# Performance work log

Hardware: AMD Instinct MI355X
Metric: run time of the kernel (lower is better)

The kernel has to match this reference:

```python
import jax, jax.numpy as jnp
import numpy as np
import math

B, T, C, H = 2, 2048, 1024, 16
HD = C // H
WINDOW = 256  # local_attn_ctx with attnblocksize=1


def setup_inputs() -> dict:
    key = jax.random.key(0)
    k1, k2, k3 = jax.random.split(key, 3)
    x = jax.random.normal(k1, (B, T, C), dtype=jnp.float32)
    Wqkv = jax.random.normal(k2, (C, 3 * C), dtype=jnp.float32) * 0.02
    bqkv = jnp.zeros((3 * C,), dtype=jnp.float32)
    Wproj = jax.random.normal(k3, (C, C), dtype=jnp.float32) * 0.02
    bproj = jnp.zeros((C,), dtype=jnp.float32)
    # 'local' block-sparse layout at token granularity: causal + sliding window
    i = np.arange(T)[:, None]
    j = np.arange(T)[None, :]
    mask = ((j <= i) & (i - j <= WINDOW)).astype(np.int32)
    return {"x": x, "Wqkv": Wqkv, "bqkv": bqkv, "Wproj": Wproj, "bproj": bproj,
            "mask": jnp.asarray(mask)}


def reference(x, Wqkv, bqkv, Wproj, bproj, mask):
    Bb, Tt, Cc = x.shape
    qkv = (x @ Wqkv + bqkv).reshape(Bb, Tt, 3, H, HD)  # [B,T,3,H,hd]
    q = jnp.transpose(qkv[:, :, 0], (0, 2, 1, 3))  # [B,H,T,hd]
    k = jnp.transpose(qkv[:, :, 1], (0, 2, 1, 3))
    v = jnp.transpose(qkv[:, :, 2], (0, 2, 1, 3))
    scale = 1.0 / math.sqrt(HD)
    att = jnp.einsum('bhqd,bhkd->bhqk', q, k) * scale  # dense T x T scores
    att = jnp.where(mask[:Tt, :Tt] == 0, -jnp.inf, att)
    att = jax.nn.softmax(att, axis=-1)
    y = jnp.einsum('bhqk,bhkd->bhqd', att, v)
    y = jnp.transpose(y, (0, 2, 1, 3)).reshape(Bb, Tt, Cc)
    return y @ Wproj + bproj
```

## Files before the change

### kernel.cpp

```cpp
#include <hip/hip_runtime.h>
#include <hip/hip_bf16.h>
#include <math.h>

typedef __bf16 bf16;
typedef __attribute__((ext_vector_type(8))) __bf16 bf16x8;
typedef __attribute__((ext_vector_type(4))) __bf16 bf16x4;
typedef __attribute__((ext_vector_type(4))) float f32x4;

#define B_  2
#define T_  2048
#define C_  1024
#define H_  16
#define HD_ 64
#define WIN_ 256

#define GLOAD16(g, l)                                                        \
  __builtin_amdgcn_global_load_lds(                                          \
      (const __attribute__((address_space(1))) void*)(g),                    \
      (__attribute__((address_space(3))) void*)(l), 16, 0, 0)

__device__ inline void bar() {
  asm volatile("" ::: "memory");
  __builtin_amdgcn_s_barrier();
  asm volatile("" ::: "memory");
}


__global__ __launch_bounds__(256) void cvt_f32_bf16_k(const float* __restrict__ in,
                                                      bf16* __restrict__ out) {
  int idx = blockIdx.x * 256 + threadIdx.x;
  const float4 v = ((const float4*)in)[idx];
  bf16x4 o;
  o[0] = (bf16)v.x; o[1] = (bf16)v.y; o[2] = (bf16)v.z; o[3] = (bf16)v.w;
  ((bf16x4*)out)[idx] = o;
}

__global__ __launch_bounds__(256) void transpose_cvt_k(const float* __restrict__ W,
                                                       bf16* __restrict__ WT,
                                                       int K, int N) {
  __shared__ float t[32][33];
  int n0 = blockIdx.x * 32, k0 = blockIdx.y * 32;
  int tx = threadIdx.x, ty = threadIdx.y;
  #pragma unroll
  for (int i = 0; i < 32; i += 8)
    t[ty + i][tx] = W[(size_t)(k0 + ty + i) * N + (n0 + tx)];
  __syncthreads();
  #pragma unroll
  for (int i = 0; i < 32; i += 8)
    WT[(size_t)(n0 + ty + i) * K + (k0 + tx)] = (bf16)t[tx][ty + i];
}


template <int MODE>
__global__ __launch_bounds__(512, 2) void gemm8p_k(const bf16* __restrict__ A,
                                                   const bf16* __restrict__ Bt,
                                                   const float* __restrict__ bias,
                                                   void* __restrict__ out0,
                                                   void* __restrict__ out1,
                                                   int M, int N, int K) {
  const int bm = blockIdx.x * 256;
  const int bn = blockIdx.y * 256;
  const int tid  = threadIdx.x;
  const int wid  = tid >> 6;
  const int lane = tid & 63;
  const int wr = wid >> 2;
  const int wc = wid & 3;
  const int lr = lane & 15;
  const int g  = lane >> 4;

  __shared__ bf16 As[2][256 * 64];
  __shared__ bf16 Bs[2][256 * 64];

  f32x4 acc[8][4] = {};

  const int sr = lane >> 3;
  const int sc = ((lane & 7) ^ sr) << 3;
  const bf16* aS = A  + (size_t)(bm + wid * 8 + sr) * K + sc;
  const bf16* bS = Bt + (size_t)(bn + wid * 8 + sr) * K + sc;

  #define STA(p_, q_, u_)                                                    \
    GLOAD16(aS + (size_t)((q_) * 64) * K + (u_) * 64,                        \
            &As[p_][((q_) * 64 + wid * 8) * 64])
  #define STB(p_, q_, u_)                                                    \
    GLOAD16(bS + (size_t)((q_) * 64) * K + (u_) * 64,                        \
            &Bs[p_][((q_) * 64 + wid * 8) * 64])

  const int NT  = K >> 6;
  const int kc0 = ((g    ) ^ (lr & 7)) << 3;
  const int kc1 = ((4 + g) ^ (lr & 7)) << 3;

  STA(0, 0, 0); STA(0, 2, 0); STA(0, 1, 0); STA(0, 3, 0);
  STB(0, 0, 0); STB(0, 1, 0); STB(0, 2, 0); STB(0, 3, 0);
  STA(1, 0, 1); STA(1, 2, 1);
  asm volatile("s_waitcnt vmcnt(2)" ::: "memory");
  __builtin_amdgcn_s_barrier();
  asm volatile("" ::: "memory");

  #define MFMA16(mb, a0_, a1_, a2_, a3_)                                     \
    do {                                                                     \
      __builtin_amdgcn_s_setprio(1);                                         \
      _Pragma("unroll")                                                      \
      for (int n = 0; n < 4; ++n) {                                          \
        acc[(mb) + 0][n] = __builtin_amdgcn_mfma_f32_16x16x32_bf16(a0_, bv[n], acc[(mb) + 0][n], 0, 0, 0); \
        acc[(mb) + 1][n] = __builtin_amdgcn_mfma_f32_16x16x32_bf16(a1_, bv[n], acc[(mb) + 1][n], 0, 0, 0); \
        acc[(mb) + 2][n] = __builtin_amdgcn_mfma_f32_16x16x32_bf16(a2_, bv[n], acc[(mb) + 2][n], 0, 0, 0); \
        acc[(mb) + 3][n] = __builtin_amdgcn_mfma_f32_16x16x32_bf16(a3_, bv[n], acc[(mb) + 3][n], 0, 0, 0); \
      }                                                                      \
      __builtin_amdgcn_s_setprio(0);                                         \
    } while (0)

  for (int u = 0; u < NT; ++u) {
    const int p  = u & 1;
    const int pn = p ^ 1;
    const bf16* Ar = &As[p][(wr * 128 + lr) * 64];
    const bf16* Br = &Bs[p][(wc * 64  + lr) * 64];
    bf16x8 bv[4], a0, a1, a2, a3;

    #pragma unroll
    for (int n = 0; n < 4; ++n) bv[n] = *(const bf16x8*)(Br + n * 1024 + kc0);
    a0 = *(const bf16x8*)(Ar + 0 * 1024 + kc0);
    a1 = *(const bf16x8*)(Ar + 1 * 1024 + kc0);
    a2 = *(const bf16x8*)(Ar + 2 * 1024 + kc0);
    a3 = *(const bf16x8*)(Ar + 3 * 1024 + kc0);
    if (u + 1 < NT) { STA(pn, 1, u + 1); STA(pn, 3, u + 1); }
    bar();
    MFMA16(0, a0, a1, a2, a3);
    if (u + 1 < NT) asm volatile("s_waitcnt vmcnt(8)" ::: "memory");
    else            asm volatile("s_waitcnt vmcnt(0)" ::: "memory");
    bar();

    a0 = *(const bf16x8*)(Ar + 4 * 1024 + kc0);
    a1 = *(const bf16x8*)(Ar + 5 * 1024 + kc0);
    a2 = *(const bf16x8*)(Ar + 6 * 1024 + kc0);
    a3 = *(const bf16x8*)(Ar + 7 * 1024 + kc0);
    if (u + 1 < NT) { STB(pn, 0, u + 1); STB(pn, 1, u + 1); }
    bar();
    MFMA16(4, a0, a1, a2, a3);
    bar();

    #pragma unroll
    for (int n = 0; n < 4; ++n) bv[n] = *(const bf16x8*)(Br + n * 1024 + kc1);
    a0 = *(const bf16x8*)(Ar + 0 * 1024 + kc1);
    a1 = *(const bf16x8*)(Ar + 1 * 1024 + kc1);
    a2 = *(const bf16x8*)(Ar + 2 * 1024 + kc1);
    a3 = *(const bf16x8*)(Ar + 3 * 1024 + kc1);
    if (u + 1 < NT) { STB(pn, 2, u + 1); STB(pn, 3, u + 1); }
    bar();
    MFMA16(0, a0, a1, a2, a3);
    bar();

    a0 = *(const bf16x8*)(Ar + 4 * 1024 + kc1);
    a1 = *(const bf16x8*)(Ar + 5 * 1024 + kc1);
    a2 = *(const bf16x8*)(Ar + 6 * 1024 + kc1);
    a3 = *(const bf16x8*)(Ar + 7 * 1024 + kc1);
    if (u + 2 < NT) { STA(p, 0, u + 2); STA(p, 2, u + 2); }
    bar();
    MFMA16(4, a0, a1, a2, a3);
    if (u + 2 < NT) asm volatile("s_waitcnt vmcnt(2)" ::: "memory");
    else            asm volatile("s_waitcnt vmcnt(0)" ::: "memory");
    bar();
  }
  #undef MFMA16
  #undef STA
  #undef STB

  const int orow = g * 4;
  #pragma unroll
  for (int n = 0; n < 4; ++n) {
    const int nbase = bn + wc * 64 + n * 16;
    const int gn = nbase + lr;
    const float bv_ = bias[gn];
    #pragma unroll
    for (int m = 0; m < 8; ++m) {
      const int gm0 = bm + wr * 128 + m * 16 + orow;
      if (MODE == 0) {
        #pragma unroll
        for (int r = 0; r < 4; ++r)
          ((float*)out0)[(size_t)(gm0 + r) * N + gn] = acc[m][n][r] + bv_;
      } else {
        if (nbase < 2 * C_) {
          #pragma unroll
          for (int r = 0; r < 4; ++r)
            ((bf16*)out0)[(size_t)(gm0 + r) * (2 * C_) + gn] = (bf16)(acc[m][n][r] + bv_);
        } else {
          const int vcol = gn - 2 * C_;
          const int h = vcol >> 6, d = vcol & 63;
          const int b = gm0 >> 11, tok = gm0 & (T_ - 1);
          bf16x4 o;
          #pragma unroll
          for (int r = 0; r < 4; ++r) o[r] = (bf16)(acc[m][n][r] + bv_);
          *(bf16x4*)&((bf16*)out1)[(((size_t)b * H_ + h) * HD_ + d) * T_ + tok] = o;
        }
      }
    }
  }
}


template <int TM, int TN, int WM, int WN, int MODE>
__global__ __launch_bounds__(WM * WN * 64, 2)
void gemm_dp_k(const bf16* __restrict__ A, const bf16* __restrict__ Bt,
               const float* __restrict__ bias,
               void* __restrict__ out0, void* __restrict__ out1,
               int M, int N, int K) {
  constexpr int NW    = WM * WN;
  constexpr int WROWS = TM / WM;
  constexpr int WCOLS = TN / WN;
  constexpr int FM    = WROWS / 16;
  constexpr int FN    = WCOLS / 16;
  constexpr int CA    = TM / 16 / NW;
  constexpr int CB    = TN / 16 / NW;

  const int bm = blockIdx.x * TM;
  const int bn = blockIdx.y * TN;
  const int tid  = threadIdx.x;
  const int wid  = tid >> 6;
  const int lane = tid & 63;
  const int wr = wid / WN;
  const int wc = wid % WN;
  const int lr = lane & 15;
  const int g  = lane >> 4;

  __shared__ bf16 As[4][TM][32];
  __shared__ bf16 Bs[4][TN][32];

  f32x4 acc[FM][FN] = {};

  const int rloc = lane >> 2;
  const int scol = (((lane & 3) ^ (rloc & 3))) * 8;
  const bf16* aSrc = A  + (size_t)(bm + wid * CA * 16 + rloc) * K + scol;
  const bf16* bSrc = Bt + (size_t)(bn + wid * CB * 16 + rloc) * K + scol;

  #define STAGE_DP(buf, kt)                                                   \
    do {                                                                      \
      _Pragma("unroll")                                                       \
      for (int i = 0; i < CA; ++i)                                            \
        GLOAD16(aSrc + (size_t)(i * 16) * K + (kt) * 32,                      \
                &As[buf][(wid * CA + i) * 16][0]);                            \
      _Pragma("unroll")                                                       \
      for (int i = 0; i < CB; ++i)                                            \
        GLOAD16(bSrc + (size_t)(i * 16) * K + (kt) * 32,                      \
                &Bs[buf][(wid * CB + i) * 16][0]);                            \
    } while (0)

  const int NT = K >> 5;
  const int kc = (g ^ (lr & 3)) * 8;

  STAGE_DP(0, 0);
  STAGE_DP(1, 1);

  for (int t = 0; t < NT; ++t) {
    const int buf = t & 3;
    if (t + 2 < NT) {
      STAGE_DP((t + 2) & 3, t + 2);
      asm volatile("s_waitcnt vmcnt(8)" ::: "memory");
    } else if (t + 1 < NT) {
      asm volatile("s_waitcnt vmcnt(4)" ::: "memory");
    } else {
      asm volatile("s_waitcnt vmcnt(0)" ::: "memory");
    }
    __builtin_amdgcn_s_barrier();
    asm volatile("" ::: "memory");

    bf16x8 af[FM], bfv[FN];
    #pragma unroll
    for (int m = 0; m < FM; ++m)
      af[m] = *(const bf16x8*)&As[buf][wr * WROWS + m * 16 + lr][kc];
    #pragma unroll
    for (int n = 0; n < FN; ++n)
      bfv[n] = *(const bf16x8*)&Bs[buf][wc * WCOLS + n * 16 + lr][kc];

    __builtin_amdgcn_s_setprio(1);
    #pragma unroll
    for (int m = 0; m < FM; ++m)
      #pragma unroll
      for (int n = 0; n < FN; ++n)
        acc[m][n] = __builtin_amdgcn_mfma_f32_16x16x32_bf16(af[m], bfv[n], acc[m][n], 0, 0, 0);
    __builtin_amdgcn_s_setprio(0);
  }
  #undef STAGE_DP

  const int orow = g * 4;
  #pragma unroll
  for (int n = 0; n < FN; ++n) {
    const int gn = bn + wc * WCOLS + n * 16 + lr;
    const float bv = bias[gn];
    #pragma unroll
    for (int m = 0; m < FM; ++m) {
      const int gm0 = bm + wr * WROWS + m * 16 + orow;
      if (MODE == 0) {
        #pragma unroll
        for (int r = 0; r < 4; ++r)
          ((float*)out0)[(size_t)(gm0 + r) * N + gn] = acc[m][n][r] + bv;
      }
    }
  }
}


__global__ __launch_bounds__(256) void attn_mfma_k(const bf16* __restrict__ qk,
                                                   const bf16* __restrict__ vt,
                                                   bf16* __restrict__ y) {
  const int q0 = blockIdx.x * 64;
  const int h  = blockIdx.y;
  const int b  = blockIdx.z;
  const int tid  = threadIdx.x;
  const int wid  = tid >> 6;
  const int lane = tid & 63;
  const int lr = lane & 15;
  const int g  = lane >> 4;

  __shared__ bf16 Ks[64][72];
  __shared__ bf16 Vs[64][72];
  __shared__ bf16 Ps[4][16][72];

  const int qrow = q0 + wid * 16 + lr;
  const bf16* qptr = qk + ((size_t)(b * T_ + qrow)) * (2 * C_) + h * HD_;
  bf16x8 qf[2];
  qf[0] = *(const bf16x8*)(qptr + g * 8);
  qf[1] = *(const bf16x8*)(qptr + 32 + g * 8);

  float m = -1e30f, l = 0.f;
  f32x4 yacc[4] = {};

  const int kt_lo = (blockIdx.x >= 4) ? (int)blockIdx.x - 4 : 0;
  for (int kt = kt_lo; kt <= (int)blockIdx.x; ++kt) {
    __syncthreads();
    #pragma unroll
    for (int i = 0; i < 2; ++i) {
      int cc = tid + i * 256;
      int rr = cc >> 3;
      int c0 = (cc & 7) * 8;
      *(bf16x8*)&Ks[rr][c0] = *(const bf16x8*)&qk[((size_t)(b * T_) + kt * 64 + rr) * (2 * C_) + C_ + h * HD_ + c0];
      *(bf16x8*)&Vs[rr][c0] = *(const bf16x8*)&vt[(((size_t)b * H_ + h) * HD_ + rr) * T_ + kt * 64 + c0];
    }
    __syncthreads();

    f32x4 sacc[4] = {};
    #pragma unroll
    for (int t = 0; t < 4; ++t)
      #pragma unroll
      for (int s = 0; s < 2; ++s)
        sacc[t] = __builtin_amdgcn_mfma_f32_16x16x32_bf16(
            *(const bf16x8*)&Ks[t * 16 + lr][s * 32 + g * 8], qf[s], sacc[t], 0, 0, 0);

    float pv[4][4];
    float rmax = -1e30f;
    #pragma unroll
    for (int t = 0; t < 4; ++t)
      #pragma unroll
      for (int r = 0; r < 4; ++r) {
        const int key = kt * 64 + t * 16 + g * 4 + r;
        const bool valid = (key <= qrow) && (qrow - key <= WIN_);
        const float sv = valid ? sacc[t][r] * 0.125f : -__builtin_inff();
        pv[t][r] = sv;
        rmax = fmaxf(rmax, sv);
      }
    rmax = fmaxf(rmax, __shfl_xor(rmax, 16));
    rmax = fmaxf(rmax, __shfl_xor(rmax, 32));

    const float mnew = fmaxf(m, rmax);
    const float alpha = __expf(m - mnew);
    m = mnew;
    float lsum = 0.f;
    #pragma unroll
    for (int t = 0; t < 4; ++t)
      #pragma unroll
      for (int r = 0; r < 4; ++r) {
        const float e = __expf(pv[t][r] - mnew);
        pv[t][r] = e;
        lsum += e;
      }
    lsum += __shfl_xor(lsum, 16);
    lsum += __shfl_xor(lsum, 32);
    l = l * alpha + lsum;

    #pragma unroll
    for (int t = 0; t < 4; ++t) {
      bf16x4 pk;
      #pragma unroll
      for (int r = 0; r < 4; ++r) pk[r] = (bf16)pv[t][r];
      *(bf16x4*)&Ps[wid][lr][t * 16 + g * 4] = pk;
    }

    float al[4];
    #pragma unroll
    for (int r = 0; r < 4; ++r) al[r] = __shfl(alpha, g * 4 + r);
    #pragma unroll
    for (int t = 0; t < 4; ++t)
      #pragma unroll
      for (int r = 0; r < 4; ++r) yacc[t][r] *= al[r];

    bf16x8 pf[2];
    pf[0] = *(const bf16x8*)&Ps[wid][lr][g * 8];
    pf[1] = *(const bf16x8*)&Ps[wid][lr][32 + g * 8];
    #pragma unroll
    for (int t = 0; t < 4; ++t)
      #pragma unroll
      for (int s = 0; s < 2; ++s)
        yacc[t] = __builtin_amdgcn_mfma_f32_16x16x32_bf16(
            pf[s], *(const bf16x8*)&Vs[t * 16 + lr][s * 32 + g * 8], yacc[t], 0, 0, 0);
  }

  float li[4];
  #pragma unroll
  for (int r = 0; r < 4; ++r) li[r] = 1.f / __shfl(l, g * 4 + r);
  #pragma unroll
  for (int t = 0; t < 4; ++t)
    #pragma unroll
    for (int r = 0; r < 4; ++r) {
      const int tok = q0 + wid * 16 + g * 4 + r;
      y[((size_t)(b * T_ + tok)) * C_ + h * HD_ + t * 16 + lr] = (bf16)(yacc[t][r] * li[r]);
    }
}


extern "C" void kernel_launch(void* const* d_in, const int* in_sizes, int n_in,
                              void* d_out, int out_size, void* d_ws, size_t ws_size,
                              hipStream_t stream) {
  const float* x     = (const float*)d_in[0];
  const float* Wqkv  = (const float*)d_in[1];
  const float* bqkv  = (const float*)d_in[2];
  const float* Wproj = (const float*)d_in[3];
  const float* bproj = (const float*)d_in[4];
  float* out = (float*)d_out;

  const size_t SZ_QK  = (size_t)B_ * T_ * 2 * C_ * sizeof(bf16);
  const size_t SZ_VT  = (size_t)B_ * H_ * HD_ * T_ * sizeof(bf16);
  const size_t SZ_XB  = (size_t)B_ * T_ * C_ * sizeof(bf16);
  const size_t SZ_WQT = (size_t)3 * C_ * C_ * sizeof(bf16);
  const size_t SZ_WPT = (size_t)C_ * C_ * sizeof(bf16);
  const size_t NEED   = SZ_QK + SZ_VT + SZ_XB + SZ_WQT + SZ_WPT + SZ_XB;
  if (ws_size < NEED) return;

  char* ws = (char*)d_ws;
  bf16* qkb    = (bf16*)(ws);
  bf16* vtb    = (bf16*)(ws + SZ_QK);
  bf16* xb     = (bf16*)(ws + SZ_QK + SZ_VT);
  bf16* wqkvT  = (bf16*)(ws + SZ_QK + SZ_VT + SZ_XB);
  bf16* wprojT = (bf16*)(ws + SZ_QK + SZ_VT + SZ_XB + SZ_WQT);
  bf16* yb     = (bf16*)(ws + SZ_QK + SZ_VT + SZ_XB + SZ_WQT + SZ_WPT);

  cvt_f32_bf16_k<<<4096, 256, 0, stream>>>(x, xb);
  transpose_cvt_k<<<dim3(3 * C_ / 32, C_ / 32), dim3(32, 8), 0, stream>>>(Wqkv, wqkvT, C_, 3 * C_);
  transpose_cvt_k<<<dim3(C_ / 32, C_ / 32), dim3(32, 8), 0, stream>>>(Wproj, wprojT, C_, C_);

  gemm8p_k<2><<<dim3((B_ * T_) / 256, (3 * C_) / 256), 512, 0, stream>>>(
      xb, wqkvT, bqkv, qkb, vtb, B_ * T_, 3 * C_, C_);

  attn_mfma_k<<<dim3(T_ / 64, H_, B_), 256, 0, stream>>>(qkb, vtb, yb);

  gemm_dp_k<128, 128, 2, 2, 0><<<dim3((B_ * T_) / 128, C_ / 128), 256, 0, stream>>>(
      yb, wprojT, bproj, out, nullptr, B_ * T_, C_, C_);
}
```

Baseline: 97.06 us.

## Retile QKV GEMM to 256x192 blocks to fill all CUs, unify staging

Shrinks the QKV projection GEMM column tile from 256 to 192, so the grid grows from 192 to 256 blocks and better matches the GPU's compute-unit count, reducing wave-quantization idle time. The split A/B staging, spread across sub-steps with partial vmcnt waits, is replaced by one 7-load-per-warp staging macro that loads the next k-tile at the start of each iteration, with a full wait at the end. The occupancy hint of 2 blocks per CU is dropped. Each block now does less reuse per loaded A tile, and the coarser wait may expose more load latency.

```diff
diff --git a/kernel.cpp b/kernel.cpp
--- a/kernel.cpp
+++ b/kernel.cpp
@@ -52,14 +52,14 @@
 
 
 template <int MODE>
-__global__ __launch_bounds__(512, 2) void gemm8p_k(const bf16* __restrict__ A,
-                                                   const bf16* __restrict__ Bt,
-                                                   const float* __restrict__ bias,
-                                                   void* __restrict__ out0,
-                                                   void* __restrict__ out1,
-                                                   int M, int N, int K) {
+__global__ __launch_bounds__(512) void gemm8p_k(const bf16* __restrict__ A,
+                                                const bf16* __restrict__ Bt,
+                                                const float* __restrict__ bias,
+                                                void* __restrict__ out0,
+                                                void* __restrict__ out1,
+                                                int M, int N, int K) {
   const int bm = blockIdx.x * 256;
-  const int bn = blockIdx.y * 256;
+  const int bn = blockIdx.y * 192;
   const int tid  = threadIdx.x;
   const int wid  = tid >> 6;
   const int lane = tid & 63;
@@ -69,38 +69,42 @@
   const int g  = lane >> 4;
 
   __shared__ bf16 As[2][256 * 64];
-  __shared__ bf16 Bs[2][256 * 64];
-
-  f32x4 acc[8][4] = {};
+  __shared__ bf16 Bs[2][192 * 64];
+
+  f32x4 acc[8][3] = {};
 
   const int sr = lane >> 3;
   const int sc = ((lane & 7) ^ sr) << 3;
-  const bf16* aS = A  + (size_t)(bm + wid * 8 + sr) * K + sc;
-  const bf16* bS = Bt + (size_t)(bn + wid * 8 + sr) * K + sc;
-
-  #define STA(p_, q_, u_)                                                    \
-    GLOAD16(aS + (size_t)((q_) * 64) * K + (u_) * 64,                        \
-            &As[p_][((q_) * 64 + wid * 8) * 64])
-  #define STB(p_, q_, u_)                                                    \
-    GLOAD16(bS + (size_t)((q_) * 64) * K + (u_) * 64,                        \
-            &Bs[p_][((q_) * 64 + wid * 8) * 64])
+
+  #define STAGE7(pn_, u_)                                                    \
+    do {                                                                     \
+      _Pragma("unroll")                                                      \
+      for (int i = 0; i < 7; ++i) {                                          \
+        const int c = wid * 7 + i;                                           \
+        if (c < 32) {                                                        \
+          GLOAD16(A + (size_t)(bm + c * 8 + sr) * K + (u_) * 64 + sc,        \
+                  &As[pn_][c * 8 * 64]);                                     \
+        } else {                                                             \
+          GLOAD16(Bt + (size_t)(bn + (c - 32) * 8 + sr) * K + (u_) * 64 + sc,\
+                  &Bs[pn_][(c - 32) * 8 * 64]);                              \
+        }                                                                    \
+      }                                                                      \
+    } while (0)
 
   const int NT  = K >> 6;
   const int kc0 = ((g    ) ^ (lr & 7)) << 3;
   const int kc1 = ((4 + g) ^ (lr & 7)) << 3;
 
-  STA(0, 0, 0); STA(0, 2, 0); STA(0, 1, 0); STA(0, 3, 0);
-  STB(0, 0, 0); STB(0, 1, 0); STB(0, 2, 0); STB(0, 3, 0);
-  STA(1, 0, 1); STA(1, 2, 1);
-  asm volatile("s_waitcnt vmcnt(2)" ::: "memory");
+  STAGE7(0, 0);
+  asm volatile("s_waitcnt vmcnt(0)" ::: "memory");
   __builtin_amdgcn_s_barrier();
   asm volatile("" ::: "memory");
 
-  #define MFMA16(mb, a0_, a1_, a2_, a3_)                                     \
+  #define MFMA12(mb, a0_, a1_, a2_, a3_)                                     \
     do {                                                                     \
       __builtin_amdgcn_s_setprio(1);                                         \
       _Pragma("unroll")                                                      \
-      for (int n = 0; n < 4; ++n) {                                          \
+      for (int n = 0; n < 3; ++n) {                                          \
         acc[(mb) + 0][n] = __builtin_amdgcn_mfma_f32_16x16x32_bf16(a0_, bv[n], acc[(mb) + 0][n], 0, 0, 0); \
         acc[(mb) + 1][n] = __builtin_amdgcn_mfma_f32_16x16x32_bf16(a1_, bv[n], acc[(mb) + 1][n], 0, 0, 0); \
         acc[(mb) + 2][n] = __builtin_amdgcn_mfma_f32_16x16x32_bf16(a2_, bv[n], acc[(mb) + 2][n], 0, 0, 0); \
@@ -113,61 +117,54 @@
     const int p  = u & 1;
     const int pn = p ^ 1;
     const bf16* Ar = &As[p][(wr * 128 + lr) * 64];
-    const bf16* Br = &Bs[p][(wc * 64  + lr) * 64];
-    bf16x8 bv[4], a0, a1, a2, a3;
-
-    #pragma unroll
-    for (int n = 0; n < 4; ++n) bv[n] = *(const bf16x8*)(Br + n * 1024 + kc0);
+    const bf16* Br = &Bs[p][(wc * 48  + lr) * 64];
+    bf16x8 bv[3], a0, a1, a2, a3;
+
+    #pragma unroll
+    for (int n = 0; n < 3; ++n) bv[n] = *(const bf16x8*)(Br + n * 1024 + kc0);
     a0 = *(const bf16x8*)(Ar + 0 * 1024 + kc0);
     a1 = *(const bf16x8*)(Ar + 1 * 1024 + kc0);
     a2 = *(const bf16x8*)(Ar + 2 * 1024 + kc0);
     a3 = *(const bf16x8*)(Ar + 3 * 1024 + kc0);
-    if (u + 1 < NT) { STA(pn, 1, u + 1); STA(pn, 3, u + 1); }
-    bar();
-    MFMA16(0, a0, a1, a2, a3);
-    if (u + 1 < NT) asm volatile("s_waitcnt vmcnt(8)" ::: "memory");
-    else            asm volatile("s_waitcnt vmcnt(0)" ::: "memory");
+    if (u + 1 < NT) STAGE7(pn, u + 1);
+    bar();
+    MFMA12(0, a0, a1, a2, a3);
     bar();
 
     a0 = *(const bf16x8*)(Ar + 4 * 1024 + kc0);
     a1 = *(const bf16x8*)(Ar + 5 * 1024 + kc0);
     a2 = *(const bf16x8*)(Ar + 6 * 1024 + kc0);
     a3 = *(const bf16x8*)(Ar + 7 * 1024 + kc0);
-    if (u + 1 < NT) { STB(pn, 0, u + 1); STB(pn, 1, u + 1); }
-    bar();
-    MFMA16(4, a0, a1, a2, a3);
-    bar();
-
-    #pragma unroll
-    for (int n = 0; n < 4; ++n) bv[n] = *(const bf16x8*)(Br + n * 1024 + kc1);
+    bar();
+    MFMA12(4, a0, a1, a2, a3);
+    bar();
+
+    #pragma unroll
+    for (int n = 0; n < 3; ++n) bv[n] = *(const bf16x8*)(Br + n * 1024 + kc1);
     a0 = *(const bf16x8*)(Ar + 0 * 1024 + kc1);
     a1 = *(const bf16x8*)(Ar + 1 * 1024 + kc1);
     a2 = *(const bf16x8*)(Ar + 2 * 1024 + kc1);
     a3 = *(const bf16x8*)(Ar + 3 * 1024 + kc1);
-    if (u + 1 < NT) { STB(pn, 2, u + 1); STB(pn, 3, u + 1); }
-    bar();
-    MFMA16(0, a0, a1, a2, a3);
+    bar();
+    MFMA12(0, a0, a1, a2, a3);
     bar();
 
     a0 = *(const bf16x8*)(Ar + 4 * 1024 + kc1);
     a1 = *(const bf16x8*)(Ar + 5 * 1024 + kc1);
     a2 = *(const bf16x8*)(Ar + 6 * 1024 + kc1);
     a3 = *(const bf16x8*)(Ar + 7 * 1024 + kc1);
-    if (u + 2 < NT) { STA(p, 0, u + 2); STA(p, 2, u + 2); }
-    bar();
-    MFMA16(4, a0, a1, a2, a3);
-    if (u + 2 < NT) asm volatile("s_waitcnt vmcnt(2)" ::: "memory");
-    else            asm volatile("s_waitcnt vmcnt(0)" ::: "memory");
+    bar();
+    MFMA12(4, a0, a1, a2, a3);
+    asm volatile("s_waitcnt vmcnt(0)" ::: "memory");
     bar();
   }
-  #undef MFMA16
-  #undef STA
-  #undef STB
+  #undef MFMA12
+  #undef STAGE7
 
   const int orow = g * 4;
   #pragma unroll
-  for (int n = 0; n < 4; ++n) {
-    const int nbase = bn + wc * 64 + n * 16;
+  for (int n = 0; n < 3; ++n) {
+    const int nbase = bn + wc * 48 + n * 16;
     const int gn = nbase + lr;
     const float bv_ = bias[gn];
     #pragma unroll
@@ -445,7 +442,7 @@
   transpose_cvt_k<<<dim3(3 * C_ / 32, C_ / 32), dim3(32, 8), 0, stream>>>(Wqkv, wqkvT, C_, 3 * C_);
   transpose_cvt_k<<<dim3(C_ / 32, C_ / 32), dim3(32, 8), 0, stream>>>(Wproj, wprojT, C_, C_);
 
-  gemm8p_k<2><<<dim3((B_ * T_) / 256, (3 * C_) / 256), 512, 0, stream>>>(
+  gemm8p_k<2><<<dim3((B_ * T_) / 256, (3 * C_) / 192), 512, 0, stream>>>(
       xb, wqkvT, bqkv, qkb, vtb, B_ * T_, 3 * C_, C_);
 
   attn_mfma_k<<<dim3(T_ / 64, H_, B_), 256, 0, stream>>>(qkb, vtb, yb);
```

After: 93.54 us. 3.6% less time.
